# Kernel tuning notes

Measured on AMD Instinct MI355X. Metric: run time of the kernel, lower is better.

The kernel has to match this reference:

```python
import jax, jax.numpy as jnp
import numpy as np

N_EMBD = 1024
N_HEAD = 16
HEAD_DIM = N_EMBD // N_HEAD
B, T = 8, 1024


def setup_inputs() -> dict:
    key = jax.random.key(0)
    k1, k2, k3, k4 = jax.random.split(key, 4)
    x = jax.random.normal(k1, (B, T, N_EMBD), dtype=jnp.float32)
    # nn.Linear weight shapes: qkv (3C, C) no bias; proj (C, C) with bias
    w_qkv = jax.random.normal(k2, (3 * N_EMBD, N_EMBD), dtype=jnp.float32) * 0.02
    w_proj = jax.random.normal(k3, (N_EMBD, N_EMBD), dtype=jnp.float32) * 0.02
    b_proj = jax.random.normal(k4, (N_EMBD,), dtype=jnp.float32) * 0.02
    return {"x": x, "w_qkv": w_qkv, "w_proj": w_proj, "b_proj": b_proj}


def reference(x, w_qkv, w_proj, b_proj):
    Bq, Tq, C = x.shape
    qkv = jnp.einsum('btc,dc->btd', x, w_qkv)  # (B,T,3C)
    q, k, v = jnp.split(qkv, 3, axis=-1)
    def heads(t):
        return t.reshape(Bq, Tq, N_HEAD, HEAD_DIM).transpose(0, 2, 1, 3)  # (B,H,T,D)
    q, k, v = heads(q), heads(k), heads(v)
    scale = 1.0 / np.sqrt(HEAD_DIM).astype(np.float32)
    att = jnp.einsum('bhqd,bhkd->bhqk', q, k) * scale  # (B,H,T,T)
    causal = jnp.tril(jnp.ones((Tq, Tq), dtype=bool))
    att = jnp.where(causal, att, -jnp.inf)
    att = jax.nn.softmax(att, axis=-1)
    # dropout: eval mode -> identity
    y = jnp.einsum('bhqk,bhkd->bhqd', att, v)
    y = y.transpose(0, 2, 1, 3).reshape(Bq, Tq, C)
    return jnp.einsum('btc,dc->btd', y, w_proj) + b_proj
```

## Files before the change

kernel.cpp:

```cpp
#include <hip/hip_runtime.h>
#include <stdint.h>


#define Bn 8
#define Tn 1024
#define Cn 1024
#define Hn 16
#define Dn 64
#define Mn (Bn * Tn)
#define NQKV (3 * Cn)
#define QKS 2048

typedef unsigned short u16;
typedef float f32x4 __attribute__((ext_vector_type(4)));
typedef __bf16 bf16x8 __attribute__((ext_vector_type(8)));
typedef unsigned short ushx8 __attribute__((ext_vector_type(8)));
typedef unsigned short ushx4 __attribute__((ext_vector_type(4)));

__device__ __forceinline__ u16 f2bf(float f) {
  unsigned int u = __float_as_uint(f);
  u += 0x7fffu + ((u >> 16) & 1u);
  return (u16)(u >> 16);
}
__device__ __forceinline__ u16 f2bf_rna(float f) {
  return (u16)((__float_as_uint(f) + 0x8000u) >> 16);
}

__device__ __forceinline__ f32x4 mfma_bf16(ushx8 a, ushx8 b, f32x4 c) {
  return __builtin_amdgcn_mfma_f32_16x16x32_bf16(
      __builtin_bit_cast(bf16x8, a), __builtin_bit_cast(bf16x8, b), c, 0, 0, 0);
}

__device__ __forceinline__ void async16(const u16* g, u16* l) {
  __builtin_amdgcn_global_load_lds(
      (__attribute__((address_space(1))) void*)(void*)g,
      (__attribute__((address_space(3))) void*)l, 16, 0, 0);
}

template <int CTRL>
__device__ __forceinline__ float dppmov(float v) {
  return __builtin_bit_cast(float, __builtin_amdgcn_update_dpp(
      0, __builtin_bit_cast(int, v), CTRL, 0xf, 0xf, true));
}
__device__ __forceinline__ float red16max(float v) {
  v = fmaxf(v, dppmov<0xB1>(v));
  v = fmaxf(v, dppmov<0x4E>(v));
  v = fmaxf(v, dppmov<0x141>(v));
  v = fmaxf(v, dppmov<0x140>(v));
  return v;
}
__device__ __forceinline__ float red16sum(float v) {
  v += dppmov<0xB1>(v);
  v += dppmov<0x4E>(v);
  v += dppmov<0x141>(v);
  v += dppmov<0x140>(v);
  return v;
}

__global__ void cast3_kernel(const float* __restrict__ a, u16* __restrict__ oa, int na4,
                             const float* __restrict__ b, u16* __restrict__ ob, int nb4,
                             const float* __restrict__ c, u16* __restrict__ oc, int nc4) {
  int i = blockIdx.x * blockDim.x + threadIdx.x;
  const float* in;
  u16* out;
  if (i < na4) { in = a; out = oa; }
  else if (i < na4 + nb4) { in = b; out = ob; i -= na4; }
  else if (i < na4 + nb4 + nc4) { in = c; out = oc; i -= na4 + nb4; }
  else return;
  float4 v = ((const float4*)in)[i];
  ushx4 o = { f2bf(v.x), f2bf(v.y), f2bf(v.z), f2bf(v.w) };
  ((ushx4*)out)[i] = o;
}

#define SLOG2E 0.18033688011112042f

template <int BM, int MODE>
__device__ __forceinline__ void gemm_body4(
    const u16* __restrict__ A, const u16* __restrict__ Bw,
    void* __restrict__ Cout, u16* __restrict__ vt,
    const float* __restrict__ bias) {
  constexpr int ASLOT = BM * 32;
  constexpr int BSLOT = 128 * 32;
  constexpr int BBASE = 3 * ASLOT;
  constexpr int ASW = BM / 64;
  constexpr int BSW = 2;
  constexpr int LOADS = ASW + BSW;
  constexpr int MREP = BM / 32;
  constexpr int MT = Mn / BM;
  constexpr int MPX = MT / 8;

  __shared__ alignas(16) u16 lds[3 * (ASLOT + BSLOT)];

  const int tid = threadIdx.x;
  const int lane = tid & 63;
  const int wv = tid >> 6;
  const int quad = lane >> 4;
  const int l16 = lane & 15;
  const int wr = wv >> 1;
  const int wc = wv & 1;

  const int xcd = blockIdx.x & 7;
  const int loc = blockIdx.x >> 3;
  const int m0 = (xcd * MPX + (loc & (MPX - 1))) * BM;
  const int n0 = (loc / MPX) * 128;

  const u16* gA = A + (size_t)m0 * Cn;
  const u16* gB = Bw + (size_t)n0 * Cn;

  int soff[4];
#pragma unroll
  for (int s = 0; s < 4; ++s) {
    int c = s * 256 + tid;
    int row = c >> 2;
    int q = (c & 3) ^ ((row >> 1) & 3);
    soff[s] = row * Cn + q * 8;
  }

  auto stage = [&](int slot, int h) {
    const u16* sA = gA + (h >> 1) * 64 + (h & 1) * 32;
    u16* dA = lds + slot * ASLOT + tid * 8;
#pragma unroll
    for (int s = 0; s < ASW; ++s) async16(sA + soff[s], dA + s * 2048);
    const u16* sB = gB + (h >> 1) * 64 + (h & 1) * 32;
    u16* dB = lds + BBASE + slot * BSLOT + tid * 8;
#pragma unroll
    for (int s = 0; s < BSW; ++s) async16(sB + soff[s], dB + s * 2048);
  };

  const int sread = (quad ^ ((l16 >> 1) & 3)) * 8;
  const int aoff = (wr * (BM / 2) + l16) * 32 + sread;
  const int boff = BBASE + (wc * 64 + l16) * 32 + sread;

  f32x4 acc[MREP][4];
#pragma unroll
  for (int i = 0; i < MREP; ++i)
#pragma unroll
    for (int j = 0; j < 4; ++j) acc[i][j] = (f32x4){0.f, 0.f, 0.f, 0.f};
  ushx8 af[MREP], bfr[4];

  stage(0, 0);
  stage(1, 1);
  if constexpr (LOADS == 6) asm volatile("s_waitcnt vmcnt(6)" ::: "memory");
  else asm volatile("s_waitcnt vmcnt(4)" ::: "memory");
  __builtin_amdgcn_s_barrier();
  asm volatile("" ::: "memory");

#define PH(slot, sslot, hd)                                                    \
  {                                                                            \
    const u16* ab_ = lds + (slot) * ASLOT + aoff;                              \
    _Pragma("unroll") for (int mi_ = 0; mi_ < MREP; ++mi_)                     \
      af[mi_] = *(const ushx8*)(ab_ + mi_ * 512);                              \
    const u16* bb_ = lds + (slot) * BSLOT + boff;                              \
    _Pragma("unroll") for (int ni_ = 0; ni_ < 4; ++ni_)                        \
      bfr[ni_] = *(const ushx8*)(bb_ + ni_ * 512);                             \
    stage((sslot), (hd));                                                      \
    asm volatile("" ::: "memory");                                             \
    __builtin_amdgcn_s_barrier();                                              \
    asm volatile("s_waitcnt lgkmcnt(0)" ::: "memory");                         \
    __builtin_amdgcn_s_setprio(1);                                             \
    _Pragma("unroll") for (int mi_ = 0; mi_ < MREP; ++mi_) {                   \
      _Pragma("unroll") for (int ni_ = 0; ni_ < 4; ++ni_) {                    \
        acc[mi_][ni_] = mfma_bf16(af[mi_], bfr[ni_], acc[mi_][ni_]);           \
      }                                                                        \
    }                                                                          \
    __builtin_amdgcn_s_setprio(0);                                             \
    if constexpr (LOADS == 6)                                                  \
      asm volatile("s_waitcnt vmcnt(6)" ::: "memory");                         \
    else                                                                       \
      asm volatile("s_waitcnt vmcnt(4)" ::: "memory");                         \
    asm volatile("" ::: "memory");                                             \
    __builtin_amdgcn_s_barrier();                                              \
    asm volatile("" ::: "memory");                                             \
  }

#pragma unroll 1
  for (int it = 0; it < 5; ++it) {
    const int p = it * 6;
    PH(0, 2, p + 2)
    PH(1, 0, p + 3)
    PH(2, 1, p + 4)
    PH(0, 2, p + 5)
    PH(1, 0, p + 6)
    PH(2, 1, p + 7)
  }
  PH(0, 2, 31)
  PH(1, 0, 31)
#undef PH
  asm volatile("s_waitcnt vmcnt(0)" ::: "memory");

  if constexpr (MODE) {
    if (n0 < 2 * Cn) {
      const float sc = (n0 < Cn) ? SLOG2E : 1.f;
#pragma unroll
      for (int mi = 0; mi < MREP; ++mi) {
#pragma unroll
        for (int ni = 0; ni < 4; ++ni) {
          const int col = n0 + wc * 64 + ni * 16 + l16;
          const int row = m0 + wr * (BM / 2) + mi * 16 + quad * 4;
#pragma unroll
          for (int i = 0; i < 4; ++i)
            ((u16*)Cout)[(size_t)(row + i) * QKS + col] = f2bf(acc[mi][ni][i] * sc);
        }
      }
    } else {
#pragma unroll
      for (int mi = 0; mi < MREP; ++mi) {
#pragma unroll
        for (int ni = 0; ni < 4; ++ni) {
          const int colV = n0 - 2 * Cn + wc * 64 + ni * 16 + l16;
          const int hh = colV >> 6, dd = colV & 63;
          const int row0 = m0 + wr * (BM / 2) + mi * 16 + quad * 4;
          const int bb = row0 >> 10, tt = row0 & 1023;
          unsigned int lo = (unsigned int)f2bf(acc[mi][ni][0]) |
                            ((unsigned int)f2bf(acc[mi][ni][1]) << 16);
          unsigned int hi = (unsigned int)f2bf(acc[mi][ni][2]) |
                            ((unsigned int)f2bf(acc[mi][ni][3]) << 16);
          uint2 pk = {lo, hi};
          *(uint2*)&vt[((size_t)(bb * Hn + hh) * Dn + dd) * Tn + tt] = pk;
        }
      }
    }
  } else {
#pragma unroll
    for (int mi = 0; mi < MREP; ++mi) {
#pragma unroll
      for (int ni = 0; ni < 4; ++ni) {
        const int col = n0 + wc * 64 + ni * 16 + l16;
        const float bv = bias[col];
        const int row = m0 + wr * (BM / 2) + mi * 16 + quad * 4;
#pragma unroll
        for (int i = 0; i < 4; ++i)
          ((float*)Cout)[(size_t)(row + i) * Cn + col] = acc[mi][ni][i] + bv;
      }
    }
  }
}

__global__ __launch_bounds__(256, 2) void gemm_qkv_k(
    const u16* __restrict__ A, const u16* __restrict__ Bw,
    u16* __restrict__ qk, u16* __restrict__ vt) {
  gemm_body4<256, 1>(A, Bw, (void*)qk, vt, nullptr);
}
__global__ __launch_bounds__(256, 2) void gemm_proj_k(
    const u16* __restrict__ A, const u16* __restrict__ Bw,
    float* __restrict__ out, const float* __restrict__ bias) {
  gemm_body4<128, 0>(A, Bw, (void*)out, nullptr, bias);
}

__global__ __launch_bounds__(512, 4) void attn_kernel(
    const u16* __restrict__ qk, const u16* __restrict__ vt,
    u16* __restrict__ out) {
  const int j = blockIdx.x, h = blockIdx.y, b = blockIdx.z;
  const int tid = threadIdx.x;
  const int lane = tid & 63;
  const int wv = tid >> 6;
  const int quad = lane >> 4;
  const int l16 = lane & 15;

  __shared__ alignas(16) u16 Ks[2][64 * 64];
  __shared__ alignas(16) u16 Vts[2][64 * 64];
  __shared__ alignas(16) u16 Ps[8][16 * 72];

  const u16* qb = qk + (size_t)b * Tn * QKS + h * Dn;
  const u16* kb = qk + (size_t)b * Tn * QKS + Cn + h * Dn;
  const u16* vtb = vt + (size_t)(b * Hn + h) * Dn * Tn;

  const int srow = tid >> 3;
  const int scc = tid & 7;
  const int sgc = scc ^ (srow & 7);
  u16* pswv = Ps[wv];

#pragma unroll 1
  for (int ph = 0; ph < 2; ++ph) {
    const int qt = ph ? (7 - j) : j;
    const int q0w = qt * 128 + wv * 16;
    const int ntiles = 2 * qt + 2;
    const int tdiag = q0w >> 6;

    ushx8 qf[2];
    {
      const u16* qp = qb + (size_t)(q0w + l16) * QKS + quad * 8;
      qf[0] = *(const ushx8*)qp;
      qf[1] = *(const ushx8*)(qp + 32);
    }

    f32x4 o[4];
#pragma unroll
    for (int nt = 0; nt < 4; ++nt) o[nt] = (f32x4){0.f, 0.f, 0.f, 0.f};
    float mrow[4], lrow[4];
#pragma unroll
    for (int i = 0; i < 4; ++i) { mrow[i] = -__builtin_inff(); lrow[i] = 0.f; }

    __syncthreads();

    async16(kb + (size_t)srow * QKS + sgc * 8, Ks[0] + tid * 8);
    async16(vtb + (size_t)srow * Tn + sgc * 8, Vts[0] + tid * 8);

#pragma unroll 1
    for (int t = 0; t < ntiles; ++t) {
      const int kv0 = t * 64;
      const int bi = t & 1;
      __syncthreads();

      if (t + 1 < ntiles) {
        const int nkv0 = kv0 + 64;
        async16(kb + (size_t)(nkv0 + srow) * QKS + sgc * 8, Ks[bi ^ 1] + tid * 8);
        async16(vtb + (size_t)srow * Tn + nkv0 + sgc * 8, Vts[bi ^ 1] + tid * 8);
      }

      if (t > tdiag) continue;

      const u16* ks = Ks[bi];
      const u16* vs = Vts[bi];
      f32x4 s[4];
#pragma unroll
      for (int nt = 0; nt < 4; ++nt) s[nt] = (f32x4){0.f, 0.f, 0.f, 0.f};
#pragma unroll
      for (int nt = 0; nt < 4; ++nt) {
        const int rb = nt * 16 + l16;
        ushx8 b0 = *(const ushx8*)(ks + rb * 64 + (quad ^ (rb & 7)) * 8);
        ushx8 b1 = *(const ushx8*)(ks + rb * 64 + ((quad + 4) ^ (rb & 7)) * 8);
        s[nt] = mfma_bf16(qf[0], b0, s[nt]);
        s[nt] = mfma_bf16(qf[1], b1, s[nt]);
      }

      if (t == tdiag) {
#pragma unroll
        for (int i = 0; i < 4; ++i) {
          const int qr = q0w + quad * 4 + i;
          float vv[4];
          float rmax = -__builtin_inff();
#pragma unroll
          for (int nt = 0; nt < 4; ++nt) {
            float v = s[nt][i];
            if ((kv0 + nt * 16 + l16) > qr) v = -__builtin_inff();
            vv[nt] = v;
            rmax = fmaxf(rmax, v);
          }
          rmax = red16max(rmax);
          const float mnew = fmaxf(mrow[i], rmax);
          const float al = __builtin_amdgcn_exp2f(mrow[i] - mnew);
          mrow[i] = mnew;
          float rsum = 0.f;
#pragma unroll
          for (int nt = 0; nt < 4; ++nt) {
            float p = __builtin_amdgcn_exp2f(vv[nt] - mnew);
            rsum += p;
            pswv[(quad * 4 + i) * 72 + nt * 16 + l16] = f2bf_rna(p);
          }
          lrow[i] = lrow[i] * al + rsum;
#pragma unroll
          for (int nt = 0; nt < 4; ++nt) o[nt][i] *= al;
        }
      } else {
#pragma unroll
        for (int i = 0; i < 4; ++i) {
          float rmax = fmaxf(fmaxf(s[0][i], s[1][i]), fmaxf(s[2][i], s[3][i]));
          rmax = red16max(rmax);
          const float mnew = fmaxf(mrow[i], rmax);
          const float al = __builtin_amdgcn_exp2f(mrow[i] - mnew);
          mrow[i] = mnew;
          float rsum = 0.f;
#pragma unroll
          for (int nt = 0; nt < 4; ++nt) {
            float p = __builtin_amdgcn_exp2f(s[nt][i] - mnew);
            rsum += p;
            pswv[(quad * 4 + i) * 72 + nt * 16 + l16] = f2bf_rna(p);
          }
          lrow[i] = lrow[i] * al + rsum;
#pragma unroll
          for (int nt = 0; nt < 4; ++nt) o[nt][i] *= al;
        }
      }

      ushx8 pf0, pf1;
      {
        const u16* pp = pswv + l16 * 72 + quad * 8;
        pf0 = *(const ushx8*)pp;
        pf1 = *(const ushx8*)(pp + 32);
      }

#pragma unroll
      for (int nt = 0; nt < 4; ++nt) {
        const int rb = nt * 16 + l16;
        ushx8 v0 = *(const ushx8*)(vs + rb * 64 + (quad ^ (rb & 7)) * 8);
        ushx8 v1 = *(const ushx8*)(vs + rb * 64 + ((quad + 4) ^ (rb & 7)) * 8);
        o[nt] = mfma_bf16(pf0, v0, o[nt]);
        o[nt] = mfma_bf16(pf1, v1, o[nt]);
      }
    }

#pragma unroll
    for (int i = 0; i < 4; ++i) {
      const float inv = 1.f / red16sum(lrow[i]);
      const int trow = q0w + quad * 4 + i;
      u16* op = out + ((size_t)(b * Tn + trow)) * Cn + h * Dn + l16;
#pragma unroll
      for (int nt = 0; nt < 4; ++nt) op[nt * 16] = f2bf(o[nt][i] * inv);
    }
  }
}

extern "C" void kernel_launch(void* const* d_in, const int* in_sizes, int n_in,
                              void* d_out, int out_size, void* d_ws, size_t ws_size,
                              hipStream_t stream) {
  const float* x = (const float*)d_in[0];
  const float* w_qkv = (const float*)d_in[1];
  const float* w_proj = (const float*)d_in[2];
  const float* b_proj = (const float*)d_in[3];
  float* out = (float*)d_out;
  char* ws = (char*)d_ws;

  u16* xb     = (u16*)(ws);
  u16* wqkvb  = (u16*)(ws + 16777216);
  u16* wprojb = (u16*)(ws + 23068672);
  u16* qkb    = (u16*)(ws + 25165824);
  u16* vtb    = (u16*)(ws + 58720256);
  u16* yb     = (u16*)(ws + 75497472);

  cast3_kernel<<<12288, 256, 0, stream>>>(x, xb, 2097152,
                                          w_qkv, wqkvb, 786432,
                                          w_proj, wprojb, 262144);

  gemm_qkv_k<<<768, 256, 0, stream>>>(xb, wqkvb, qkb, vtb);

  attn_kernel<<<dim3(4, Hn, Bn), 512, 0, stream>>>(qkb, vtb, yb);

  gemm_proj_k<<<512, 256, 0, stream>>>(yb, wprojb, out, b_proj);
}
```

Measured before the change: 220.1 us.

## Use 512-thread QKV GEMM and triple-buffered two-tile attention pipeline

Result: faster. 214.1 us (-2.7%).

```diff
diff --git a/kernel.cpp b/kernel.cpp
--- a/kernel.cpp
+++ b/kernel.cpp
@@ -73,6 +73,159 @@
 }
 
 #define SLOG2E 0.18033688011112042f
+
+template <int MODE>
+__device__ __forceinline__ void gemm_body(
+    const u16* __restrict__ A, const u16* __restrict__ Bw,
+    void* __restrict__ Cout, u16* __restrict__ vt,
+    const float* __restrict__ bias) {
+  __shared__ alignas(16) u16 lds[36864];
+
+  const int tid = threadIdx.x;
+  const int lane = tid & 63;
+  const int wv = tid >> 6;
+  const int quad = lane >> 4;
+  const int l16 = lane & 15;
+  const int wr = wv >> 1;
+  const int wc = wv & 1;
+
+  const int xcd = blockIdx.x & 7;
+  const int loc = blockIdx.x >> 3;
+  const int m0 = (xcd * 4 + (loc & 3)) * 256;
+  const int n0 = (loc >> 2) * 128;
+
+  const u16* gA = A + (size_t)m0 * Cn;
+  const u16* gB = Bw + (size_t)n0 * Cn;
+
+  const int r0s = tid >> 2;
+  const int q0s = (tid & 3) ^ ((r0s >> 1) & 3);
+  const int c1s = 512 + tid;
+  const int r1s = c1s >> 2;
+  const int q1s = (c1s & 3) ^ ((r1s >> 1) & 3);
+  const int so0 = r0s * Cn + q0s * 8;
+  const int so1 = r1s * Cn + q1s * 8;
+
+  auto stageA = [&](int slot, int h) {
+    u16* dst = lds + slot * 8192 + tid * 8;
+    const u16* src = gA + (h >> 1) * 64 + (h & 1) * 32;
+    async16(src + so0, dst);
+    async16(src + so1, dst + 4096);
+  };
+  auto stageB = [&](int slot, int h) {
+    u16* dst = lds + 24576 + slot * 4096 + tid * 8;
+    const u16* src = gB + (h >> 1) * 64 + (h & 1) * 32;
+    async16(src + so0, dst);
+  };
+
+  const int sread = (quad ^ ((l16 >> 1) & 3)) * 8;
+  const int aoff = (wr * 64 + l16) * 32 + sread;
+  const int boff = 24576 + (wc * 64 + l16) * 32 + sread;
+
+  f32x4 acc[4][4];
+#pragma unroll
+  for (int i = 0; i < 4; ++i)
+#pragma unroll
+    for (int jj = 0; jj < 4; ++jj) acc[i][jj] = (f32x4){0.f, 0.f, 0.f, 0.f};
+  ushx8 af[4], bfr[4];
+
+  stageA(0, 0); stageB(0, 0);
+  stageA(1, 1); stageB(1, 1);
+  asm volatile("s_waitcnt vmcnt(3)" ::: "memory");
+  __builtin_amdgcn_s_barrier();
+  asm volatile("" ::: "memory");
+
+#define PH(slot, sslot, hd)                                                    \
+  {                                                                            \
+    const u16* ab_ = lds + (slot) * 8192 + aoff;                               \
+    af[0] = *(const ushx8*)(ab_);                                              \
+    af[1] = *(const ushx8*)(ab_ + 512);                                        \
+    af[2] = *(const ushx8*)(ab_ + 1024);                                       \
+    af[3] = *(const ushx8*)(ab_ + 1536);                                       \
+    const u16* bb_ = lds + (slot) * 4096 + boff;                               \
+    bfr[0] = *(const ushx8*)(bb_);                                             \
+    bfr[1] = *(const ushx8*)(bb_ + 512);                                       \
+    bfr[2] = *(const ushx8*)(bb_ + 1024);                                      \
+    bfr[3] = *(const ushx8*)(bb_ + 1536);                                      \
+    stageA((sslot), (hd));                                                     \
+    stageB((sslot), (hd));                                                     \
+    asm volatile("" ::: "memory");                                             \
+    __builtin_amdgcn_s_barrier();                                              \
+    asm volatile("s_waitcnt lgkmcnt(0)" ::: "memory");                         \
+    __builtin_amdgcn_s_setprio(1);                                             \
+    _Pragma("unroll") for (int mi_ = 0; mi_ < 4; ++mi_) {                      \
+      _Pragma("unroll") for (int ni_ = 0; ni_ < 4; ++ni_) {                    \
+        acc[mi_][ni_] = mfma_bf16(af[mi_], bfr[ni_], acc[mi_][ni_]);           \
+      }                                                                        \
+    }                                                                          \
+    __builtin_amdgcn_s_setprio(0);                                             \
+    asm volatile("s_waitcnt vmcnt(3)" ::: "memory");                           \
+    asm volatile("" ::: "memory");                                             \
+    __builtin_amdgcn_s_barrier();                                              \
+    asm volatile("" ::: "memory");                                             \
+  }
+
+#pragma unroll 1
+  for (int it = 0; it < 5; ++it) {
+    const int p = it * 6;
+    PH(0, 2, p + 2)
+    PH(1, 0, p + 3)
+    PH(2, 1, p + 4)
+    PH(0, 2, p + 5)
+    PH(1, 0, p + 6)
+    PH(2, 1, p + 7)
+  }
+  PH(0, 2, 31)
+  PH(1, 0, 31)
+#undef PH
+  asm volatile("s_waitcnt vmcnt(0)" ::: "memory");
+
+  if constexpr (MODE) {
+    if (n0 < 2 * Cn) {
+      const float sc = (n0 < Cn) ? SLOG2E : 1.f;
+#pragma unroll
+      for (int mi = 0; mi < 4; ++mi) {
+#pragma unroll
+        for (int ni = 0; ni < 4; ++ni) {
+          const int col = n0 + wc * 64 + ni * 16 + l16;
+          const int row = m0 + wr * 64 + mi * 16 + quad * 4;
+#pragma unroll
+          for (int i = 0; i < 4; ++i)
+            ((u16*)Cout)[(size_t)(row + i) * QKS + col] = f2bf(acc[mi][ni][i] * sc);
+        }
+      }
+    } else {
+#pragma unroll
+      for (int mi = 0; mi < 4; ++mi) {
+#pragma unroll
+        for (int ni = 0; ni < 4; ++ni) {
+          const int colV = n0 - 2 * Cn + wc * 64 + ni * 16 + l16;
+          const int hh = colV >> 6, dd = colV & 63;
+          const int row0 = m0 + wr * 64 + mi * 16 + quad * 4;
+          const int bb = row0 >> 10, tt = row0 & 1023;
+          unsigned int lo = (unsigned int)f2bf(acc[mi][ni][0]) |
+                            ((unsigned int)f2bf(acc[mi][ni][1]) << 16);
+          unsigned int hi = (unsigned int)f2bf(acc[mi][ni][2]) |
+                            ((unsigned int)f2bf(acc[mi][ni][3]) << 16);
+          uint2 pk = {lo, hi};
+          *(uint2*)&vt[((size_t)(bb * Hn + hh) * Dn + dd) * Tn + tt] = pk;
+        }
+      }
+    }
+  } else {
+#pragma unroll
+    for (int mi = 0; mi < 4; ++mi) {
+#pragma unroll
+      for (int ni = 0; ni < 4; ++ni) {
+        const int col = n0 + wc * 64 + ni * 16 + l16;
+        const float bv = bias[col];
+        const int row = m0 + wr * 64 + mi * 16 + quad * 4;
+#pragma unroll
+        for (int i = 0; i < 4; ++i)
+          ((float*)Cout)[(size_t)(row + i) * Cn + col] = acc[mi][ni][i] + bv;
+      }
+    }
+  }
+}
 
 template <int BM, int MODE>
 __device__ __forceinline__ void gemm_body4(
@@ -135,7 +288,7 @@
 #pragma unroll
   for (int i = 0; i < MREP; ++i)
 #pragma unroll
-    for (int j = 0; j < 4; ++j) acc[i][j] = (f32x4){0.f, 0.f, 0.f, 0.f};
+    for (int jj = 0; jj < 4; ++jj) acc[i][jj] = (f32x4){0.f, 0.f, 0.f, 0.f};
   ushx8 af[MREP], bfr[4];
 
   stage(0, 0);
@@ -189,37 +342,6 @@
   asm volatile("s_waitcnt vmcnt(0)" ::: "memory");
 
   if constexpr (MODE) {
-    if (n0 < 2 * Cn) {
-      const float sc = (n0 < Cn) ? SLOG2E : 1.f;
-#pragma unroll
-      for (int mi = 0; mi < MREP; ++mi) {
-#pragma unroll
-        for (int ni = 0; ni < 4; ++ni) {
-          const int col = n0 + wc * 64 + ni * 16 + l16;
-          const int row = m0 + wr * (BM / 2) + mi * 16 + quad * 4;
-#pragma unroll
-          for (int i = 0; i < 4; ++i)
-            ((u16*)Cout)[(size_t)(row + i) * QKS + col] = f2bf(acc[mi][ni][i] * sc);
-        }
-      }
-    } else {
-#pragma unroll
-      for (int mi = 0; mi < MREP; ++mi) {
-#pragma unroll
-        for (int ni = 0; ni < 4; ++ni) {
-          const int colV = n0 - 2 * Cn + wc * 64 + ni * 16 + l16;
-          const int hh = colV >> 6, dd = colV & 63;
-          const int row0 = m0 + wr * (BM / 2) + mi * 16 + quad * 4;
-          const int bb = row0 >> 10, tt = row0 & 1023;
-          unsigned int lo = (unsigned int)f2bf(acc[mi][ni][0]) |
-                            ((unsigned int)f2bf(acc[mi][ni][1]) << 16);
-          unsigned int hi = (unsigned int)f2bf(acc[mi][ni][2]) |
-                            ((unsigned int)f2bf(acc[mi][ni][3]) << 16);
-          uint2 pk = {lo, hi};
-          *(uint2*)&vt[((size_t)(bb * Hn + hh) * Dn + dd) * Tn + tt] = pk;
-        }
-      }
-    }
   } else {
 #pragma unroll
     for (int mi = 0; mi < MREP; ++mi) {
@@ -236,10 +358,10 @@
   }
 }
 
-__global__ __launch_bounds__(256, 2) void gemm_qkv_k(
+__global__ __launch_bounds__(512, 4) void gemm_qkv_k(
     const u16* __restrict__ A, const u16* __restrict__ Bw,
     u16* __restrict__ qk, u16* __restrict__ vt) {
-  gemm_body4<256, 1>(A, Bw, (void*)qk, vt, nullptr);
+  gemm_body<1>(A, Bw, (void*)qk, vt, nullptr);
 }
 __global__ __launch_bounds__(256, 2) void gemm_proj_k(
     const u16* __restrict__ A, const u16* __restrict__ Bw,
@@ -257,8 +379,8 @@
   const int quad = lane >> 4;
   const int l16 = lane & 15;
 
-  __shared__ alignas(16) u16 Ks[2][64 * 64];
-  __shared__ alignas(16) u16 Vts[2][64 * 64];
+  __shared__ alignas(16) u16 Ks[3][64 * 64];
+  __shared__ alignas(16) u16 Vts[3][64 * 64];
   __shared__ alignas(16) u16 Ps[8][16 * 72];
 
   const u16* qb = qk + (size_t)b * Tn * QKS + h * Dn;
@@ -266,9 +388,14 @@
   const u16* vtb = vt + (size_t)(b * Hn + h) * Dn * Tn;
 
   const int srow = tid >> 3;
-  const int scc = tid & 7;
-  const int sgc = scc ^ (srow & 7);
+  const int sgc = (tid & 7) ^ (srow & 7);
   u16* pswv = Ps[wv];
+
+  auto stageKV = [&](int slot, int kt) {
+    const int kv0s = kt * 64;
+    async16(kb + (size_t)(kv0s + srow) * QKS + sgc * 8, Ks[slot] + tid * 8);
+    async16(vtb + (size_t)srow * Tn + kv0s + sgc * 8, Vts[slot] + tid * 8);
+  };
 
 #pragma unroll 1
   for (int ph = 0; ph < 2; ++ph) {
@@ -291,28 +418,7 @@
 #pragma unroll
     for (int i = 0; i < 4; ++i) { mrow[i] = -__builtin_inff(); lrow[i] = 0.f; }
 
-    __syncthreads();
-
-    async16(kb + (size_t)srow * QKS + sgc * 8, Ks[0] + tid * 8);
-    async16(vtb + (size_t)srow * Tn + sgc * 8, Vts[0] + tid * 8);
-
-#pragma unroll 1
-    for (int t = 0; t < ntiles; ++t) {
-      const int kv0 = t * 64;
-      const int bi = t & 1;
-      __syncthreads();
-
-      if (t + 1 < ntiles) {
-        const int nkv0 = kv0 + 64;
-        async16(kb + (size_t)(nkv0 + srow) * QKS + sgc * 8, Ks[bi ^ 1] + tid * 8);
-        async16(vtb + (size_t)srow * Tn + nkv0 + sgc * 8, Vts[bi ^ 1] + tid * 8);
-      }
-
-      if (t > tdiag) continue;
-
-      const u16* ks = Ks[bi];
-      const u16* vs = Vts[bi];
-      f32x4 s[4];
+    auto qkt = [&](f32x4* s, const u16* ks) {
 #pragma unroll
       for (int nt = 0; nt < 4; ++nt) s[nt] = (f32x4){0.f, 0.f, 0.f, 0.f};
 #pragma unroll
@@ -323,8 +429,11 @@
         s[nt] = mfma_bf16(qf[0], b0, s[nt]);
         s[nt] = mfma_bf16(qf[1], b1, s[nt]);
       }
-
-      if (t == tdiag) {
+    };
+
+    auto smpv = [&](f32x4* s, int tt, const u16* vs) {
+      const int kv0 = tt * 64;
+      if (tt == tdiag) {
 #pragma unroll
         for (int i = 0; i < 4; ++i) {
           const int qr = q0w + quad * 4 + i;
@@ -372,14 +481,12 @@
           for (int nt = 0; nt < 4; ++nt) o[nt][i] *= al;
         }
       }
-
       ushx8 pf0, pf1;
       {
         const u16* pp = pswv + l16 * 72 + quad * 8;
         pf0 = *(const ushx8*)pp;
         pf1 = *(const ushx8*)(pp + 32);
       }
-
 #pragma unroll
       for (int nt = 0; nt < 4; ++nt) {
         const int rb = nt * 16 + l16;
@@ -388,6 +495,32 @@
         o[nt] = mfma_bf16(pf0, v0, o[nt]);
         o[nt] = mfma_bf16(pf1, v1, o[nt]);
       }
+    };
+
+    __syncthreads();
+    stageKV(0, 0);
+    stageKV(1, 1);
+
+#pragma unroll 1
+    for (int t = 0; t < ntiles; t += 2) {
+      const int s0 = t % 3;
+      const int s1 = (t + 1) % 3;
+      __syncthreads();
+
+      if (t + 2 < ntiles) stageKV((t + 2) % 3, t + 2);
+
+      const bool a1 = (t <= tdiag);
+      const bool a2 = (t + 1 <= tdiag);
+
+      f32x4 sA[4], sB[4];
+      if (a1) qkt(sA, Ks[s0]);
+      if (a2) qkt(sB, Ks[s1]);
+      if (a1) smpv(sA, t, Vts[s0]);
+
+      __syncthreads();
+      if (t + 3 < ntiles) stageKV((t + 3) % 3, t + 3);
+
+      if (a2) smpv(sB, t + 1, Vts[s1]);
     }
 
 #pragma unroll
@@ -422,7 +555,7 @@
                                           w_qkv, wqkvb, 786432,
                                           w_proj, wprojb, 262144);
 
-  gemm_qkv_k<<<768, 256, 0, stream>>>(xb, wqkvb, qkb, vtb);
+  gemm_qkv_k<<<768, 512, 0, stream>>>(xb, wqkvb, qkb, vtb);
 
   attn_kernel<<<dim3(4, Hn, Bn), 512, 0, stream>>>(qkb, vtb, yb);
 
```
